# Kernel tuning notes

Hardware: AMD Instinct MI355X
Metric: run time of the kernel (lower is better)

The kernel has to match this reference:

```python
import jax, jax.numpy as jnp
from jax import lax
import numpy as np

ALPHA = 2.0
EROSIONS = 10


def setup_inputs() -> dict:
    key = jax.random.key(0)
    k1, k2 = jax.random.split(key)
    b, c, h, w = 32, 1, 1024, 1024
    pred = jax.random.uniform(k1, (b, c, h, w), dtype=jnp.float32)
    target = jax.random.randint(k2, (b, c, h, w), 0, 2, dtype=jnp.int32)
    return {"pred": pred, "target": target}


def _perform_erosion(bound, kernel, alpha, erosions):
    # bound: (b, 1, H, W); kernel: (1, 1, 3, 3) cross * 0.2
    def step(carry, k):
        bnd, eroted = carry
        dilation = lax.conv_general_dilated(bnd, kernel, window_strides=(1, 1), padding="SAME")
        erosion = jnp.maximum(dilation - 0.5, 0.0)
        # per-sample global max/min over channel+spatial dims
        emax = jnp.max(erosion, axis=(1, 2, 3), keepdims=True)
        emin = jnp.min(erosion, axis=(1, 2, 3), keepdims=True)
        denom = emax - emin
        safe = jnp.where(denom != 0, denom, jnp.ones_like(denom))
        erosion = jnp.where(denom != 0, (erosion - emin) / safe, erosion)
        eroted = eroted + erosion * (k + 1.0) ** alpha
        return (erosion, eroted), None

    init = (bound, jnp.zeros_like(bound))
    (_, eroted), _ = lax.scan(step, init, jnp.arange(erosions, dtype=bound.dtype))
    return eroted


def reference(pred, target):
    # cross-shaped 3x3 erosion kernel scaled by 0.2 (fixed buffer)
    cross = jnp.array([[0.0, 1.0, 0.0], [1.0, 1.0, 1.0], [0.0, 1.0, 0.0]], dtype=pred.dtype) * 0.2
    kernel = cross[None, None]  # (1, 1, 3, 3)
    c = pred.shape[1]
    losses = []
    for i in range(c):
        tgt = (target == i).astype(pred.dtype)  # (b, c, H, W); c==1 here
        bound = (pred[:, i : i + 1] - tgt) ** 2
        eroted = _perform_erosion(bound, kernel, ALPHA, EROSIONS)
        losses.append(jnp.mean(eroted))
    return jnp.mean(jnp.stack(losses))
```

## Files before the change

kernel.cpp:

```cpp
#include <hip/hip_runtime.h>
#include <hip/hip_fp16.h>

#define BATCH 32
#define H 1024
#define W 1024
#define NPIX (H * W)
#define ITERS 10
#define SROWS 8
#define BROWS 16
#define STRIPS (H / BROWS)

typedef _Float16 half8_t __attribute__((ext_vector_type(8)));

struct Stats {
    unsigned maxbits[ITERS][BATCH];
    unsigned minbits[ITERS][BATCH];
    double   sum[ITERS][BATCH];
};

__global__ void init_stats(Stats* st) {
    int i = blockIdx.x * blockDim.x + threadIdx.x;
    if (i < ITERS * BATCH) {
        (&st->maxbits[0][0])[i] = 0u;
        (&st->minbits[0][0])[i] = 0x7f800000u;
        (&st->sum[0][0])[i]     = 0.0;
    }
}

__device__ __forceinline__ float bound1(const float* __restrict__ pred,
                                        const int* __restrict__ tgt, size_t off) {
    float d = pred[off] - (tgt[off] == 0 ? 1.f : 0.f);
    return d * d;
}

template <int MODE>
__device__ __forceinline__ void row_load8(
    const float* __restrict__ pred, const int* __restrict__ target,
    const _Float16* __restrict__ in, size_t base, int r, int lane128,
    float emin, float invd, float f[8], float& L, float& R)
{
    const int  col = lane128 * 8;
    const bool inb = (r >= 0) && (r < H);
    size_t off = base + (size_t)r * W + col;
    if (inb) {
        if (MODE == 0) {
            float4 p0 = *(const float4*)(pred + off);
            float4 p1 = *(const float4*)(pred + off + 4);
            int4   t0 = *(const int4*)(target + off);
            int4   t1 = *(const int4*)(target + off + 4);
            float d;
            d = p0.x - (t0.x == 0 ? 1.f : 0.f); f[0] = d * d;
            d = p0.y - (t0.y == 0 ? 1.f : 0.f); f[1] = d * d;
            d = p0.z - (t0.z == 0 ? 1.f : 0.f); f[2] = d * d;
            d = p0.w - (t0.w == 0 ? 1.f : 0.f); f[3] = d * d;
            d = p1.x - (t1.x == 0 ? 1.f : 0.f); f[4] = d * d;
            d = p1.y - (t1.y == 0 ? 1.f : 0.f); f[5] = d * d;
            d = p1.z - (t1.z == 0 ? 1.f : 0.f); f[6] = d * d;
            d = p1.w - (t1.w == 0 ? 1.f : 0.f); f[7] = d * d;
        } else {
            half8_t x = *(const half8_t*)(in + off);
            #pragma unroll
            for (int j = 0; j < 8; ++j)
                f[j] = ((float)x[j] - emin) * invd;
        }
    } else {
        #pragma unroll
        for (int j = 0; j < 8; ++j) f[j] = 0.f;
    }

    L = __shfl_up(f[7], 1, 64);
    R = __shfl_down(f[0], 1, 64);

    const int wl = lane128 & 63;
    if (!inb) { L = 0.f; R = 0.f; return; }
    if (lane128 == 0) {
        L = 0.f;
    } else if (wl == 0) {
        size_t o = off - 1;
        L = (MODE == 0) ? bound1(pred, target, o)
                        : ((float)in[o] - emin) * invd;
    }
    if (lane128 == 127) {
        R = 0.f;
    } else if (wl == 63) {
        size_t o = off + 8;
        R = (MODE == 0) ? bound1(pred, target, o)
                        : ((float)in[o] - emin) * invd;
    }
}

template <int MODE, int STORE>
__global__ __launch_bounds__(256) void erode_strip(
    const float* __restrict__ pred, const int* __restrict__ target,
    const _Float16* __restrict__ in, _Float16* __restrict__ out,
    Stats* __restrict__ st, int iter)
{
    const int blk = blockIdx.x;
    const int b   = blk >> 6;
    const int s   = blk & (STRIPS - 1);
    const int tid = threadIdx.x;
    const int sub     = tid >> 7;
    const int lane128 = tid & 127;
    const int r0  = s * BROWS + sub * SROWS;
    const int col = lane128 * 8;
    const size_t base = (size_t)b * NPIX;

    float emin = 0.f, invd = 1.f;
    if (MODE == 1) {
        float emax = __uint_as_float(st->maxbits[iter - 1][b]);
        float emn  = __uint_as_float(st->minbits[iter - 1][b]);
        float denom = emax - emn;
        if (denom != 0.f) { emin = emn; invd = 1.f / denom; }
    }

    float prev[8], cur[8], nxt[8];
    float Lp, Rp, Lc, Rc, Ln, Rn;
    row_load8<MODE>(pred, target, in, base, r0 - 1, lane128, emin, invd, prev, Lp, Rp);
    row_load8<MODE>(pred, target, in, base, r0,     lane128, emin, invd, cur,  Lc, Rc);

    float  m  = 0.f;
    float  mn = __builtin_inf();
    double sum = 0.0;

    #pragma unroll 2
    for (int i = 0; i < SROWS; ++i) {
        const int r = r0 + i;
        row_load8<MODE>(pred, target, in, base, r + 1, lane128, emin, invd, nxt, Ln, Rn);

        float e[8];
        #pragma unroll
        for (int j = 0; j < 8; ++j) {
            float lf = (j == 0) ? Lc : cur[j - 1];
            float rf = (j == 7) ? Rc : cur[j + 1];
            e[j] = fmaxf(0.2f * (cur[j] + lf + rf + prev[j] + nxt[j]) - 0.5f, 0.f);
        }

        if (STORE) {
            half8_t o;
            #pragma unroll
            for (int j = 0; j < 8; ++j) o[j] = (_Float16)e[j];
            *(half8_t*)(out + base + (size_t)r * W + col) = o;
        }

        float rm = fmaxf(fmaxf(fmaxf(e[0], e[1]), fmaxf(e[2], e[3])),
                         fmaxf(fmaxf(e[4], e[5]), fmaxf(e[6], e[7])));
        float rn = fminf(fminf(fminf(e[0], e[1]), fminf(e[2], e[3])),
                         fminf(fminf(e[4], e[5]), fminf(e[6], e[7])));
        float rs = ((e[0] + e[1]) + (e[2] + e[3])) + ((e[4] + e[5]) + (e[6] + e[7]));
        m   = fmaxf(m, rm);
        mn  = fminf(mn, rn);
        sum += (double)rs;

        #pragma unroll
        for (int j = 0; j < 8; ++j) { prev[j] = cur[j]; cur[j] = nxt[j]; }
        Lc = Ln; Rc = Rn;
    }

    #pragma unroll
    for (int off = 32; off > 0; off >>= 1) {
        m   = fmaxf(m,  __shfl_down(m,  off, 64));
        mn  = fminf(mn, __shfl_down(mn, off, 64));
        sum += __shfl_down(sum, off, 64);
    }
    __shared__ float  smax[4];
    __shared__ float  smin[4];
    __shared__ double ssum[4];
    int lane = tid & 63, wave = tid >> 6;
    if (lane == 0) { smax[wave] = m; smin[wave] = mn; ssum[wave] = sum; }
    __syncthreads();
    if (tid == 0) {
        m   = fmaxf(fmaxf(smax[0], smax[1]), fmaxf(smax[2], smax[3]));
        mn  = fminf(fminf(smin[0], smin[1]), fminf(smin[2], smin[3]));
        sum = ssum[0] + ssum[1] + ssum[2] + ssum[3];
        atomicMax(&st->maxbits[iter][b], __float_as_uint(m));
        atomicMin(&st->minbits[iter][b], __float_as_uint(mn));
        atomicAdd(&st->sum[iter][b], sum);
    }
}

__global__ void finalize(const Stats* __restrict__ st, float* __restrict__ out) {
    if (threadIdx.x == 0 && blockIdx.x == 0) {
        double total = 0.0;
        for (int k = 0; k < ITERS; ++k) {
            double w = (double)((k + 1) * (k + 1));
            for (int b = 0; b < BATCH; ++b) {
                float emax  = __uint_as_float(st->maxbits[k][b]);
                float emn   = __uint_as_float(st->minbits[k][b]);
                float denom = emax - emn;
                double s = st->sum[k][b];
                double sn;
                if (denom != 0.f)
                    sn = (s - (double)NPIX * (double)emn) / (double)denom;
                else
                    sn = s;
                total += w * sn;
            }
        }
        out[0] = (float)(total / ((double)BATCH * (double)NPIX));
    }
}

extern "C" void kernel_launch(void* const* d_in, const int* in_sizes, int n_in,
                              void* d_out, int out_size, void* d_ws, size_t ws_size,
                              hipStream_t stream) {
    (void)in_sizes; (void)n_in; (void)out_size;
    const float* pred   = (const float*)d_in[0];
    const int*   target = (const int*)d_in[1];

    const size_t fieldBytes = (size_t)BATCH * NPIX * sizeof(_Float16);
    char* ws = (char*)d_ws;
    _Float16* bufA;
    _Float16* bufB;
    Stats* st;
    if (ws_size >= 2 * fieldBytes + sizeof(Stats)) {
        bufA = (_Float16*)ws;
        bufB = (_Float16*)(ws + fieldBytes);
        st   = (Stats*)(ws + 2 * fieldBytes);
    } else {
        bufA = (_Float16*)ws;
        bufB = (_Float16*)d_in[1];
        st   = (Stats*)(ws + fieldBytes);
    }

    init_stats<<<1, 320, 0, stream>>>(st);

    dim3 grid(BATCH * STRIPS), block(256);
    erode_strip<0, 1><<<grid, block, 0, stream>>>(pred, target, nullptr, bufA, st, 0);

    _Float16* src = bufA;
    _Float16* dst = bufB;
    for (int k = 1; k < ITERS; ++k) {
        if (k == ITERS - 1)
            erode_strip<1, 0><<<grid, block, 0, stream>>>(nullptr, nullptr, src, dst, st, k);
        else
            erode_strip<1, 1><<<grid, block, 0, stream>>>(nullptr, nullptr, src, dst, st, k);
        _Float16* t = src; src = dst; dst = t;
    }

    finalize<<<1, 64, 0, stream>>>(st, (float*)d_out);
}
```

Before: 646.3 us.

## Fuse all erosion iterations into one persistent kernel with register-resident fields

Replaces the ten per-iteration strip launches with a single persistent kernel of 512 blocks. Each thread keeps its 32-row by 8-column slice of the fp16 field in registers across iterations. Only boundary rows are exchanged, through a small halo buffer in global memory and shared memory, and a software grid barrier after each iteration makes the per-sample min/max available. This removes the full-field global read and write per iteration and the launch overhead. In exchange it depends on all 512 blocks being co-resident, since the spin barrier deadlocks otherwise, and it carries heavy register pressure from the 32 half8 registers per thread.

```diff
diff --git a/kernel.cpp b/kernel.cpp
--- a/kernel.cpp
+++ b/kernel.cpp
@@ -1,14 +1,14 @@
 #include <hip/hip_runtime.h>
-#include <hip/hip_fp16.h>
 
 #define BATCH 32
 #define H 1024
 #define W 1024
 #define NPIX (H * W)
 #define ITERS 10
-#define SROWS 8
-#define BROWS 16
-#define STRIPS (H / BROWS)
+#define STRIPS 16
+#define BROWS 64
+#define SROWS 32
+#define NBLK (BATCH * STRIPS)
 
 typedef _Float16 half8_t __attribute__((ext_vector_type(8)));
 
@@ -18,13 +18,18 @@
     double   sum[ITERS][BATCH];
 };
 
-__global__ void init_stats(Stats* st) {
+__global__ void init_all(Stats* st, unsigned* bar) {
     int i = blockIdx.x * blockDim.x + threadIdx.x;
     if (i < ITERS * BATCH) {
         (&st->maxbits[0][0])[i] = 0u;
         (&st->minbits[0][0])[i] = 0x7f800000u;
         (&st->sum[0][0])[i]     = 0.0;
     }
+    if (i == 0) *bar = 0u;
+}
+
+__device__ __forceinline__ size_t halo_off(int parity, int b, int s, int side) {
+    return ((((size_t)parity * BATCH + b) * STRIPS + s) * 2 + side) * W;
 }
 
 __device__ __forceinline__ float bound1(const float* __restrict__ pred,
@@ -33,148 +38,235 @@
     return d * d;
 }
 
-template <int MODE>
-__device__ __forceinline__ void row_load8(
-    const float* __restrict__ pred, const int* __restrict__ target,
-    const _Float16* __restrict__ in, size_t base, int r, int lane128,
-    float emin, float invd, float f[8], float& L, float& R)
+__device__ __forceinline__ void bound_row(const float* __restrict__ pred,
+                                          const int* __restrict__ target,
+                                          size_t base, int r, int lane128,
+                                          float f[8], float& L, float& R)
 {
     const int  col = lane128 * 8;
     const bool inb = (r >= 0) && (r < H);
     size_t off = base + (size_t)r * W + col;
     if (inb) {
-        if (MODE == 0) {
-            float4 p0 = *(const float4*)(pred + off);
-            float4 p1 = *(const float4*)(pred + off + 4);
-            int4   t0 = *(const int4*)(target + off);
-            int4   t1 = *(const int4*)(target + off + 4);
-            float d;
-            d = p0.x - (t0.x == 0 ? 1.f : 0.f); f[0] = d * d;
-            d = p0.y - (t0.y == 0 ? 1.f : 0.f); f[1] = d * d;
-            d = p0.z - (t0.z == 0 ? 1.f : 0.f); f[2] = d * d;
-            d = p0.w - (t0.w == 0 ? 1.f : 0.f); f[3] = d * d;
-            d = p1.x - (t1.x == 0 ? 1.f : 0.f); f[4] = d * d;
-            d = p1.y - (t1.y == 0 ? 1.f : 0.f); f[5] = d * d;
-            d = p1.z - (t1.z == 0 ? 1.f : 0.f); f[6] = d * d;
-            d = p1.w - (t1.w == 0 ? 1.f : 0.f); f[7] = d * d;
-        } else {
-            half8_t x = *(const half8_t*)(in + off);
-            #pragma unroll
-            for (int j = 0; j < 8; ++j)
-                f[j] = ((float)x[j] - emin) * invd;
-        }
+        float4 p0 = *(const float4*)(pred + off);
+        float4 p1 = *(const float4*)(pred + off + 4);
+        int4   t0 = *(const int4*)(target + off);
+        int4   t1 = *(const int4*)(target + off + 4);
+        float d;
+        d = p0.x - (t0.x == 0 ? 1.f : 0.f); f[0] = d * d;
+        d = p0.y - (t0.y == 0 ? 1.f : 0.f); f[1] = d * d;
+        d = p0.z - (t0.z == 0 ? 1.f : 0.f); f[2] = d * d;
+        d = p0.w - (t0.w == 0 ? 1.f : 0.f); f[3] = d * d;
+        d = p1.x - (t1.x == 0 ? 1.f : 0.f); f[4] = d * d;
+        d = p1.y - (t1.y == 0 ? 1.f : 0.f); f[5] = d * d;
+        d = p1.z - (t1.z == 0 ? 1.f : 0.f); f[6] = d * d;
+        d = p1.w - (t1.w == 0 ? 1.f : 0.f); f[7] = d * d;
     } else {
         #pragma unroll
         for (int j = 0; j < 8; ++j) f[j] = 0.f;
     }
-
     L = __shfl_up(f[7], 1, 64);
     R = __shfl_down(f[0], 1, 64);
-
-    const int wl = lane128 & 63;
     if (!inb) { L = 0.f; R = 0.f; return; }
-    if (lane128 == 0) {
-        L = 0.f;
-    } else if (wl == 0) {
-        size_t o = off - 1;
-        L = (MODE == 0) ? bound1(pred, target, o)
-                        : ((float)in[o] - emin) * invd;
-    }
-    if (lane128 == 127) {
-        R = 0.f;
-    } else if (wl == 63) {
-        size_t o = off + 8;
-        R = (MODE == 0) ? bound1(pred, target, o)
-                        : ((float)in[o] - emin) * invd;
-    }
-}
-
-template <int MODE, int STORE>
-__global__ __launch_bounds__(256) void erode_strip(
+    if (lane128 == 0)                 L = 0.f;
+    else if ((lane128 & 63) == 0)     L = bound1(pred, target, off - 1);
+    if (lane128 == 127)               R = 0.f;
+    else if ((lane128 & 63) == 63)    R = bound1(pred, target, off + 8);
+}
+
+__device__ __forceinline__ void norm8(float f[8], half8_t v, float emin, float invd) {
+    #pragma unroll
+    for (int j = 0; j < 8; ++j) f[j] = ((float)v[j] - emin) * invd;
+}
+
+__device__ __forceinline__ void zero8(float f[8]) {
+    #pragma unroll
+    for (int j = 0; j < 8; ++j) f[j] = 0.f;
+}
+
+__device__ __forceinline__ half8_t pack8(const float e[8]) {
+    half8_t o;
+    #pragma unroll
+    for (int j = 0; j < 8; ++j) o[j] = (_Float16)e[j];
+    return o;
+}
+
+__device__ __forceinline__ void conv_row(const float prev[8], const float cur[8],
+                                         const float nxt[8], float Lc, float Rc,
+                                         float e[8])
+{
+    #pragma unroll
+    for (int j = 0; j < 8; ++j) {
+        float lf = (j == 0) ? Lc : cur[j - 1];
+        float rf = (j == 7) ? Rc : cur[j + 1];
+        e[j] = fmaxf(0.2f * (cur[j] + lf + rf + prev[j] + nxt[j]) - 0.5f, 0.f);
+    }
+}
+
+__device__ __forceinline__ void grid_barrier(unsigned* bar, int epoch) {
+    __threadfence();
+    __syncthreads();
+    if (threadIdx.x == 0) {
+        atomicAdd(bar, 1u);
+        unsigned tgt = (unsigned)NBLK * (unsigned)(epoch + 1);
+        while (__hip_atomic_load(bar, __ATOMIC_RELAXED, __HIP_MEMORY_SCOPE_AGENT) < tgt) {
+            __builtin_amdgcn_s_sleep(2);
+        }
+    }
+    __syncthreads();
+    __threadfence();
+}
+
+__global__ __launch_bounds__(256, 2) void erode_persist(
     const float* __restrict__ pred, const int* __restrict__ target,
-    const _Float16* __restrict__ in, _Float16* __restrict__ out,
-    Stats* __restrict__ st, int iter)
+    _Float16* __restrict__ halo, Stats* __restrict__ st, unsigned* __restrict__ bar)
 {
     const int blk = blockIdx.x;
-    const int b   = blk >> 6;
+    const int b   = blk >> 4;
     const int s   = blk & (STRIPS - 1);
     const int tid = threadIdx.x;
     const int sub     = tid >> 7;
     const int lane128 = tid & 127;
+    const int col = lane128 * 8;
     const int r0  = s * BROWS + sub * SROWS;
-    const int col = lane128 * 8;
     const size_t base = (size_t)b * NPIX;
-
-    float emin = 0.f, invd = 1.f;
-    if (MODE == 1) {
-        float emax = __uint_as_float(st->maxbits[iter - 1][b]);
-        float emn  = __uint_as_float(st->minbits[iter - 1][b]);
-        float denom = emax - emn;
-        if (denom != 0.f) { emin = emn; invd = 1.f / denom; }
-    }
-
-    float prev[8], cur[8], nxt[8];
-    float Lp, Rp, Lc, Rc, Ln, Rn;
-    row_load8<MODE>(pred, target, in, base, r0 - 1, lane128, emin, invd, prev, Lp, Rp);
-    row_load8<MODE>(pred, target, in, base, r0,     lane128, emin, invd, cur,  Lc, Rc);
-
-    float  m  = 0.f;
-    float  mn = __builtin_inf();
-    double sum = 0.0;
-
-    #pragma unroll 2
-    for (int i = 0; i < SROWS; ++i) {
-        const int r = r0 + i;
-        row_load8<MODE>(pred, target, in, base, r + 1, lane128, emin, invd, nxt, Ln, Rn);
-
-        float e[8];
-        #pragma unroll
-        for (int j = 0; j < 8; ++j) {
-            float lf = (j == 0) ? Lc : cur[j - 1];
-            float rf = (j == 7) ? Rc : cur[j + 1];
-            e[j] = fmaxf(0.2f * (cur[j] + lf + rf + prev[j] + nxt[j]) - 0.5f, 0.f);
-        }
-
-        if (STORE) {
-            half8_t o;
-            #pragma unroll
-            for (int j = 0; j < 8; ++j) o[j] = (_Float16)e[j];
-            *(half8_t*)(out + base + (size_t)r * W + col) = o;
-        }
-
-        float rm = fmaxf(fmaxf(fmaxf(e[0], e[1]), fmaxf(e[2], e[3])),
-                         fmaxf(fmaxf(e[4], e[5]), fmaxf(e[6], e[7])));
-        float rn = fminf(fminf(fminf(e[0], e[1]), fminf(e[2], e[3])),
-                         fminf(fminf(e[4], e[5]), fminf(e[6], e[7])));
-        float rs = ((e[0] + e[1]) + (e[2] + e[3])) + ((e[4] + e[5]) + (e[6] + e[7]));
-        m   = fmaxf(m, rm);
-        mn  = fminf(mn, rn);
-        sum += (double)rs;
-
-        #pragma unroll
-        for (int j = 0; j < 8; ++j) { prev[j] = cur[j]; cur[j] = nxt[j]; }
-        Lc = Ln; Rc = Rn;
-    }
-
-    #pragma unroll
-    for (int off = 32; off > 0; off >>= 1) {
-        m   = fmaxf(m,  __shfl_down(m,  off, 64));
-        mn  = fminf(mn, __shfl_down(mn, off, 64));
-        sum += __shfl_down(sum, off, 64);
-    }
+    const int lane = tid & 63, wave = tid >> 6;
+
+    __shared__ _Float16 vrow[2][W];
+    __shared__ _Float16 bcolL[2][SROWS];
+    __shared__ _Float16 bcolR[2][SROWS];
     __shared__ float  smax[4];
     __shared__ float  smin[4];
     __shared__ double ssum[4];
-    int lane = tid & 63, wave = tid >> 6;
-    if (lane == 0) { smax[wave] = m; smin[wave] = mn; ssum[wave] = sum; }
-    __syncthreads();
-    if (tid == 0) {
-        m   = fmaxf(fmaxf(smax[0], smax[1]), fmaxf(smax[2], smax[3]));
-        mn  = fminf(fminf(smin[0], smin[1]), fminf(smin[2], smin[3]));
-        sum = ssum[0] + ssum[1] + ssum[2] + ssum[3];
-        atomicMax(&st->maxbits[iter][b], __float_as_uint(m));
-        atomicMin(&st->minbits[iter][b], __float_as_uint(mn));
-        atomicAdd(&st->sum[iter][b], sum);
+
+    half8_t fld[SROWS];
+
+    float prev[8], cur[8], nxt[8], e[8];
+    float Lc, Rc, Ln, Rn;
+    float m, mn;
+    double sum;
+
+    {
+        float Lp, Rp;
+        bound_row(pred, target, base, r0 - 1, lane128, prev, Lp, Rp);
+        bound_row(pred, target, base, r0,     lane128, cur,  Lc, Rc);
+        m = 0.f; mn = __uint_as_float(0x7f800000u); sum = 0.0;
+        #pragma unroll
+        for (int i = 0; i < SROWS; ++i) {
+            bound_row(pred, target, base, r0 + i + 1, lane128, nxt, Ln, Rn);
+            conv_row(prev, cur, nxt, Lc, Rc, e);
+            fld[i] = pack8(e);
+            float rm = fmaxf(fmaxf(fmaxf(e[0], e[1]), fmaxf(e[2], e[3])),
+                             fmaxf(fmaxf(e[4], e[5]), fmaxf(e[6], e[7])));
+            float rn = fminf(fminf(fminf(e[0], e[1]), fminf(e[2], e[3])),
+                             fminf(fminf(e[4], e[5]), fminf(e[6], e[7])));
+            float rs = ((e[0] + e[1]) + (e[2] + e[3])) + ((e[4] + e[5]) + (e[6] + e[7]));
+            m = fmaxf(m, rm); mn = fminf(mn, rn); sum += (double)rs;
+            #pragma unroll
+            for (int j = 0; j < 8; ++j) { prev[j] = cur[j]; cur[j] = nxt[j]; }
+            Lc = Ln; Rc = Rn;
+        }
+    }
+
+    for (int k = 0; k < ITERS; ++k) {
+        if (k < ITERS - 1) {
+            _Float16* ho = halo + halo_off((k + 1) & 1, b, s, sub) + col;
+            *(half8_t*)ho = (sub == 0) ? fld[0] : fld[SROWS - 1];
+        }
+        {
+            float rm = m, rn = mn; double rs = sum;
+            #pragma unroll
+            for (int off = 32; off > 0; off >>= 1) {
+                rm = fmaxf(rm, __shfl_down(rm, off, 64));
+                rn = fminf(rn, __shfl_down(rn, off, 64));
+                rs += __shfl_down(rs, off, 64);
+            }
+            if (lane == 0) { smax[wave] = rm; smin[wave] = rn; ssum[wave] = rs; }
+            __syncthreads();
+            if (tid == 0) {
+                rm = fmaxf(fmaxf(smax[0], smax[1]), fmaxf(smax[2], smax[3]));
+                rn = fminf(fminf(smin[0], smin[1]), fminf(smin[2], smin[3]));
+                rs = ssum[0] + ssum[1] + ssum[2] + ssum[3];
+                atomicMax(&st->maxbits[k][b], __float_as_uint(rm));
+                atomicMin(&st->minbits[k][b], __float_as_uint(rn));
+                atomicAdd(&st->sum[k][b], rs);
+            }
+        }
+        if (k == ITERS - 1) break;
+        grid_barrier(bar, k);
+
+        float emax  = __uint_as_float(st->maxbits[k][b]);
+        float emn   = __uint_as_float(st->minbits[k][b]);
+        float denom = emax - emn;
+        float emin = 0.f, invd = 1.f;
+        if (denom != 0.f) { emin = emn; invd = 1.f / denom; }
+
+        {
+            _Float16* vr = &vrow[sub == 0 ? 0 : 1][col];
+            *(half8_t*)vr = (sub == 0) ? fld[SROWS - 1] : fld[0];
+            if (lane128 == 63) {
+                #pragma unroll
+                for (int i = 0; i < SROWS; ++i) bcolL[sub][i] = fld[i][7];
+            }
+            if (lane128 == 64) {
+                #pragma unroll
+                for (int i = 0; i < SROWS; ++i) bcolR[sub][i] = fld[i][0];
+            }
+        }
+        __syncthreads();
+
+        const int pin = (k + 1) & 1;
+        if (sub == 0) {
+            if (s > 0) {
+                half8_t hr = *(const half8_t*)(halo + halo_off(pin, b, s - 1, 1) + col);
+                norm8(prev, hr, emin, invd);
+            } else zero8(prev);
+        } else {
+            half8_t hr = *(const half8_t*)(&vrow[0][col]);
+            norm8(prev, hr, emin, invd);
+        }
+        {
+            norm8(cur, fld[0], emin, invd);
+            Lc = __shfl_up(cur[7], 1, 64);
+            Rc = __shfl_down(cur[0], 1, 64);
+            if (lane128 == 0)        Lc = 0.f;
+            else if (lane128 == 64)  Lc = ((float)bcolL[sub][0] - emin) * invd;
+            if (lane128 == 127)      Rc = 0.f;
+            else if (lane128 == 63)  Rc = ((float)bcolR[sub][0] - emin) * invd;
+        }
+
+        m = 0.f; mn = __uint_as_float(0x7f800000u); sum = 0.0;
+        #pragma unroll
+        for (int i = 0; i < SROWS; ++i) {
+            if (i < SROWS - 1) {
+                norm8(nxt, fld[i + 1], emin, invd);
+                Ln = __shfl_up(nxt[7], 1, 64);
+                Rn = __shfl_down(nxt[0], 1, 64);
+                if (lane128 == 0)        Ln = 0.f;
+                else if (lane128 == 64)  Ln = ((float)bcolL[sub][i + 1] - emin) * invd;
+                if (lane128 == 127)      Rn = 0.f;
+                else if (lane128 == 63)  Rn = ((float)bcolR[sub][i + 1] - emin) * invd;
+            } else {
+                if (sub == 0) {
+                    half8_t hr = *(const half8_t*)(&vrow[1][col]);
+                    norm8(nxt, hr, emin, invd);
+                } else if (s < STRIPS - 1) {
+                    half8_t hr = *(const half8_t*)(halo + halo_off(pin, b, s + 1, 0) + col);
+                    norm8(nxt, hr, emin, invd);
+                } else zero8(nxt);
+                Ln = 0.f; Rn = 0.f;
+            }
+            conv_row(prev, cur, nxt, Lc, Rc, e);
+            fld[i] = pack8(e);
+            float rm = fmaxf(fmaxf(fmaxf(e[0], e[1]), fmaxf(e[2], e[3])),
+                             fmaxf(fmaxf(e[4], e[5]), fmaxf(e[6], e[7])));
+            float rn = fminf(fminf(fminf(e[0], e[1]), fminf(e[2], e[3])),
+                             fminf(fminf(e[4], e[5]), fminf(e[6], e[7])));
+            float rs = ((e[0] + e[1]) + (e[2] + e[3])) + ((e[4] + e[5]) + (e[6] + e[7]));
+            m = fmaxf(m, rm); mn = fminf(mn, rn); sum += (double)rs;
+            #pragma unroll
+            for (int j = 0; j < 8; ++j) { prev[j] = cur[j]; cur[j] = nxt[j]; }
+            Lc = Ln; Rc = Rn;
+        }
     }
 }
 
@@ -187,12 +279,12 @@
                 float emax  = __uint_as_float(st->maxbits[k][b]);
                 float emn   = __uint_as_float(st->minbits[k][b]);
                 float denom = emax - emn;
-                double s = st->sum[k][b];
+                double ssv = st->sum[k][b];
                 double sn;
                 if (denom != 0.f)
-                    sn = (s - (double)NPIX * (double)emn) / (double)denom;
+                    sn = (ssv - (double)NPIX * (double)emn) / (double)denom;
                 else
-                    sn = s;
+                    sn = ssv;
                 total += w * sn;
             }
         }
@@ -203,39 +295,16 @@
 extern "C" void kernel_launch(void* const* d_in, const int* in_sizes, int n_in,
                               void* d_out, int out_size, void* d_ws, size_t ws_size,
                               hipStream_t stream) {
-    (void)in_sizes; (void)n_in; (void)out_size;
+    (void)in_sizes; (void)n_in; (void)out_size; (void)ws_size;
     const float* pred   = (const float*)d_in[0];
     const int*   target = (const int*)d_in[1];
 
-    const size_t fieldBytes = (size_t)BATCH * NPIX * sizeof(_Float16);
     char* ws = (char*)d_ws;
-    _Float16* bufA;
-    _Float16* bufB;
-    Stats* st;
-    if (ws_size >= 2 * fieldBytes + sizeof(Stats)) {
-        bufA = (_Float16*)ws;
-        bufB = (_Float16*)(ws + fieldBytes);
-        st   = (Stats*)(ws + 2 * fieldBytes);
-    } else {
-        bufA = (_Float16*)ws;
-        bufB = (_Float16*)d_in[1];
-        st   = (Stats*)(ws + fieldBytes);
-    }
-
-    init_stats<<<1, 320, 0, stream>>>(st);
-
-    dim3 grid(BATCH * STRIPS), block(256);
-    erode_strip<0, 1><<<grid, block, 0, stream>>>(pred, target, nullptr, bufA, st, 0);
-
-    _Float16* src = bufA;
-    _Float16* dst = bufB;
-    for (int k = 1; k < ITERS; ++k) {
-        if (k == ITERS - 1)
-            erode_strip<1, 0><<<grid, block, 0, stream>>>(nullptr, nullptr, src, dst, st, k);
-        else
-            erode_strip<1, 1><<<grid, block, 0, stream>>>(nullptr, nullptr, src, dst, st, k);
-        _Float16* t = src; src = dst; dst = t;
-    }
-
+    Stats*    st   = (Stats*)ws;
+    unsigned* bar  = (unsigned*)(ws + 8192);
+    _Float16* halo = (_Float16*)(ws + 65536);
+
+    init_all<<<2, 256, 0, stream>>>(st, bar);
+    erode_persist<<<NBLK, 256, 0, stream>>>(pred, target, halo, st, bar);
     finalize<<<1, 64, 0, stream>>>(st, (float*)d_out);
 }
```

New measurement: 1.507 ms. 133% more time.
